# Performance work log

Measured on AMD Instinct MI355X. Metric: run time of the kernel, lower is better.

The kernel has to match this reference:

```python
import jax, jax.numpy as jnp
import numpy as np

EPS = 1e-5  # BatchNorm1d default eps

def _conv1d(x, w, stride, pad):
    # x: [B, Cin, L], w: [Cout, Cin, K]
    return jax.lax.conv_general_dilated(
        x, w, window_strides=(stride,), padding=[(pad, pad)],
        dimension_numbers=('NCH', 'OIH', 'NCH'))

def _bn(x, g, b, m, v):
    # eval-mode BatchNorm1d with running stats; x: [B, C, L]
    scale = g / jnp.sqrt(v + EPS)
    return x * scale[None, :, None] + (b - m * scale)[None, :, None]

def _hardtanh(x):
    return jnp.clip(x, -1.0, 1.0)

def _maxpool2(x):
    B, C, L = x.shape
    return x.reshape(B, C, L // 2, 2).max(axis=-1)


def setup_inputs() -> dict:
    key = jax.random.key(0)
    ks = jax.random.split(key, 20)
    B, L = 256, 16384
    x = jax.random.normal(ks[0], (B, 1, L), dtype=jnp.float32)
    rms = jax.random.uniform(ks[1], (B, 1), dtype=jnp.float32)
    # conv weights (fan-in scaled)
    w1 = jax.random.normal(ks[2], (16, 1, 17), dtype=jnp.float32) * (1.0 / np.sqrt(1 * 17))
    w2 = jax.random.normal(ks[3], (32, 16, 9), dtype=jnp.float32) * (1.0 / np.sqrt(16 * 9))
    w3 = jax.random.normal(ks[4], (64, 32, 5), dtype=jnp.float32) * (1.0 / np.sqrt(32 * 5))
    # batchnorm params (eval mode: gamma, beta, running mean/var)
    def bn_params(k, C):
        k1, k2, k3, k4 = jax.random.split(k, 4)
        g = 1.0 + 0.1 * jax.random.normal(k1, (C,), dtype=jnp.float32)
        b = 0.1 * jax.random.normal(k2, (C,), dtype=jnp.float32)
        m = 0.1 * jax.random.normal(k3, (C,), dtype=jnp.float32)
        v = jax.random.uniform(k4, (C,), dtype=jnp.float32, minval=0.5, maxval=1.5)
        return g, b, m, v
    g1, b1, m1, v1 = bn_params(ks[5], 16)
    g2, b2, m2, v2 = bn_params(ks[6], 32)
    g3, b3, m3, v3 = bn_params(ks[7], 64)
    fc1_w = jax.random.normal(ks[8], (32, 65), dtype=jnp.float32) * (1.0 / np.sqrt(65))
    fc1_b = jnp.zeros((32,), dtype=jnp.float32)
    fc2_w = jax.random.normal(ks[9], (2, 32), dtype=jnp.float32) * (1.0 / np.sqrt(32))
    fc2_b = jnp.zeros((2,), dtype=jnp.float32)
    return dict(x=x, rms=rms, w1=w1, g1=g1, b1=b1, m1=m1, v1=v1,
                w2=w2, g2=g2, b2=b2, m2=m2, v2=v2,
                w3=w3, g3=g3, b3=b3, m3=m3, v3=v3,
                fc1_w=fc1_w, fc1_b=fc1_b, fc2_w=fc2_w, fc2_b=fc2_b)


def reference(x, rms, w1, g1, b1, m1, v1, w2, g2, b2, m2, v2,
              w3, g3, b3, m3, v3, fc1_w, fc1_b, fc2_w, fc2_b):
    # Stage 1: float conv
    h = _conv1d(x, w1, 2, 8)                 # [B,16,8192]
    h = _maxpool2(_hardtanh(_bn(h, g1, b1, m1, v1)))  # [B,16,4096]
    # Stage 2: binarized (sign) weight conv
    h = _conv1d(h, jnp.sign(w2), 2, 4)       # [B,32,2048]
    h = _maxpool2(_hardtanh(_bn(h, g2, b2, m2, v2)))  # [B,32,1024]
    # Stage 3: binarized weight conv
    h = _conv1d(h, jnp.sign(w3), 2, 2)       # [B,64,512]
    h = _maxpool2(_hardtanh(_bn(h, g3, b3, m3, v3)))  # [B,64,256]
    feat = h.mean(axis=-1)                   # AdaptiveAvgPool1d(1) -> [B,64]
    combined = jnp.concatenate([feat, rms], axis=1)   # [B,65]
    h = _hardtanh(combined @ fc1_w.T + fc1_b)
    return h @ fc2_w.T + fc2_b               # [B,2]
```

## Files before the change

### kernel.cpp

```cpp
#include <hip/hip_runtime.h>
#include <hip/hip_bf16.h>

#define EPS 1e-5f

typedef float f32x4 __attribute__((ext_vector_type(4)));
typedef short s16x8 __attribute__((ext_vector_type(8)));

union FragU { uint4 u; s16x8 s; };

__device__ __forceinline__ float ht(float x){ return __builtin_amdgcn_fmed3f(x, -1.f, 1.f); }
__device__ __forceinline__ float sgn(float v){ return (v>0.f)?1.f:((v<0.f)?-1.f:0.f); }
__device__ __forceinline__ unsigned short f2bf(float f){
    unsigned int u = __builtin_bit_cast(unsigned int, f);
    u += 0x7FFFu + ((u>>16)&1u);
    return (unsigned short)(u>>16);
}
__device__ __forceinline__ unsigned pkbf(float a, float b){
    __hip_bfloat162 h = __float22bfloat162_rn(float2{a, b});
    unsigned u;
    __builtin_memcpy(&u, &h, sizeof(u));
    return u;
}

__global__ __launch_bounds__(512) void prep(
    const float* __restrict__ w1, const float* __restrict__ w2, const float* __restrict__ w3,
    const float* g1,const float* b1,const float* m1,const float* v1,
    const float* g2,const float* b2,const float* m2,const float* v2,
    const float* g3,const float* b3,const float* m3,const float* v3,
    unsigned short* __restrict__ a1, unsigned short* __restrict__ a2,
    unsigned short* __restrict__ a3, float* __restrict__ bn){
  const int t = threadIdx.x, bid = blockIdx.x;
  if(bid == 0){
    if(t < 64){
      int q = t>>4, m = t&15;
      #pragma unroll
      for(int j=0;j<8;++j){ int k = 8*q+j;
        a1[t*8+j] = f2bf((k<17)? w1[m*17+k] : 0.f); }
    }
    if(t<16){ float s = g1[t]*rsqrtf(v1[t]+EPS); bn[t]    = s; bn[16+t]  = b1[t]-m1[t]*s; }
    if(t<32){ float s = g2[t]*rsqrtf(v2[t]+EPS); bn[32+t] = s; bn[64+t]  = b2[t]-m2[t]*s; }
    if(t<64){ float s = g3[t]*rsqrtf(v3[t]+EPS); bn[96+t] = s; bn[160+t] = b3[t]-m3[t]*s; }
  } else if(bid <= 2){
    int e = (bid-1)*512 + t;
    if(e < 640){
      int m = e&15, q = (e>>4)&3, hc = e>>6, c = hc%5, h = hc/5;
      int oc = m + 16*h, k = 2*c + (q>>1);
      #pragma unroll
      for(int j=0;j<8;++j){ int ic = 8*(q&1)+j;
        a2[e*8+j] = f2bf((k<9)? sgn(w2[(oc*16+ic)*9+k]) : 0.f); }
    }
  } else {
    int e = (bid-3)*512 + t;
    if(e < 1280){
      int m = e&15, q = (e>>4)&3, gc = e>>6, c = gc%5, g = gc/5;
      int oc = m + 16*g;
      #pragma unroll
      for(int j=0;j<8;++j){ int ic = 8*q+j;
        a3[e*8+j] = f2bf(sgn(w3[(oc*32+ic)*5+c])); }
    }
  }
}

__global__ __launch_bounds__(256, 4) void kfused(const float* __restrict__ x,
    const unsigned short* __restrict__ a1, const unsigned short* __restrict__ a2,
    const unsigned short* __restrict__ a3, const float* __restrict__ bn,
    float* __restrict__ partial){
  __shared__ __align__(16) unsigned short xs[1216];
  __shared__ __align__(16) unsigned short s1[296*24];
  __shared__ __align__(16) unsigned short s2[68*40];
  __shared__ float fws[4*32];
  const int b  = blockIdx.x >> 4;
  const int t  = blockIdx.x & 15;
  const int Q0 = 16*t;
  const int tid = threadIdx.x;
  const int m = tid & 15, q = (tid & 63) >> 4, w = tid >> 6;

  const int x0 = 64*Q0 - 56;
  const float* xrow = &x[b*16384];
  for(int i = tid; i < 304; i += 256){
    int g0 = x0 + 4*i;
    float4 v = make_float4(0.f,0.f,0.f,0.f);
    if(g0 >= 0 && g0 <= 16380) v = *(const float4*)&xrow[g0];
    uint2 pk;
    pk.x = pkbf(v.x, v.y);
    pk.y = pkbf(v.z, v.w);
    *(uint2*)&xs[4*i] = pk;
  }
  FragU af1; af1.u = *(const uint4*)&a1[(q*16+m)*8];
  const float sc1 = bn[m], sh1 = bn[16+m];
  __syncthreads();

  const unsigned* X32 = (const unsigned*)xs;
  for(int it = 0; it < 10; ++it){
    int tile = it*4 + w;
    if(tile < 37){
      int d = tile*16 + m + 4*q;
      FragU bf;
      bf.u.x = X32[d]; bf.u.y = X32[d+1]; bf.u.z = X32[d+2]; bf.u.w = X32[d+3];
      f32x4 acc = {0.f,0.f,0.f,0.f};
      acc = __builtin_amdgcn_mfma_f32_16x16x32_bf16(bf.s, af1.s, acc, 0,0,0);
      float v0 = ht(acc[0]*sc1 + sh1);
      float v1 = ht(acc[1]*sc1 + sh1);
      float v2 = ht(acc[2]*sc1 + sh1);
      float v3 = ht(acc[3]*sc1 + sh1);
      int ppl = tile*8 + 2*q;
      int gp  = 16*Q0 - 12 + ppl;
      float p0 = ((unsigned)gp     < 4096u) ? fmaxf(v0, v1) : 0.f;
      float p1 = ((unsigned)(gp+1) < 4096u) ? fmaxf(v2, v3) : 0.f;
      unsigned u = pkbf(p0, p1);
      s1[ppl*24 + m]     = (unsigned short)u;
      s1[(ppl+1)*24 + m] = (unsigned short)(u >> 16);
    }
  }
  __syncthreads();

  FragU af2[2][5];
  #pragma unroll
  for(int h=0;h<2;++h)
    #pragma unroll
    for(int c=0;c<5;++c)
      af2[h][c].u = *(const uint4*)&a2[(((h*5+c)*4+q)*16+m)*8];
  float sc2[2], sh2[2];
  #pragma unroll
  for(int h=0;h<2;++h){
    sc2[h] = bn[32 + m + 16*h];
    sh2[h] = bn[64 + m + 16*h];
  }
  for(int it = 0; it < 3; ++it){
    int tile = it*4 + w;
    if(tile < 9){
      int nl = tile*16 + m;
      f32x4 acc[2] = {{0.f,0.f,0.f,0.f},{0.f,0.f,0.f,0.f}};
      #pragma unroll
      for(int c=0;c<5;++c){
        int row = 2*nl + 2*c + (q>>1);
        FragU bf; bf.u = *(const uint4*)&s1[row*24 + 8*(q&1)];
        acc[0] = __builtin_amdgcn_mfma_f32_16x16x32_bf16(bf.s, af2[0][c].s, acc[0],0,0,0);
        acc[1] = __builtin_amdgcn_mfma_f32_16x16x32_bf16(bf.s, af2[1][c].s, acc[1],0,0,0);
      }
      int ppl = tile*8 + 2*q;
      int gp  = 4*Q0 - 2 + ppl;
      bool ok0 = (unsigned)gp     < 1024u;
      bool ok1 = (unsigned)(gp+1) < 1024u;
      #pragma unroll
      for(int h=0;h<2;++h){
        float v0 = ht(acc[h][0]*sc2[h] + sh2[h]);
        float v1 = ht(acc[h][1]*sc2[h] + sh2[h]);
        float v2 = ht(acc[h][2]*sc2[h] + sh2[h]);
        float v3 = ht(acc[h][3]*sc2[h] + sh2[h]);
        float p0 = ok0 ? fmaxf(v0, v1) : 0.f;
        float p1 = ok1 ? fmaxf(v2, v3) : 0.f;
        unsigned u = pkbf(p0, p1);
        if(ppl < 68){
          s2[ppl*40 + m + 16*h]     = (unsigned short)u;
          s2[(ppl+1)*40 + m + 16*h] = (unsigned short)(u >> 16);
        }
      }
    }
  }
  __syncthreads();

  const int tw = w & 1, gw = w >> 1;
  FragU af3[2][5];
  #pragma unroll
  for(int gl=0;gl<2;++gl)
    #pragma unroll
    for(int c=0;c<5;++c)
      af3[gl][c].u = *(const uint4*)&a3[((((2*gw+gl)*5+c)*4+q)*16+m)*8];
  float sc3[2], sh3[2];
  #pragma unroll
  for(int gl=0;gl<2;++gl){
    sc3[gl] = bn[96  + m + 16*(2*gw+gl)];
    sh3[gl] = bn[160 + m + 16*(2*gw+gl)];
  }
  {
    int nl = tw*16 + m;
    f32x4 acc[2] = {{0.f,0.f,0.f,0.f},{0.f,0.f,0.f,0.f}};
    #pragma unroll
    for(int c=0;c<5;++c){
      int row = 2*nl + c;
      FragU bf; bf.u = *(const uint4*)&s2[row*40 + 8*q];
      acc[0] = __builtin_amdgcn_mfma_f32_16x16x32_bf16(bf.s, af3[0][c].s, acc[0],0,0,0);
      acc[1] = __builtin_amdgcn_mfma_f32_16x16x32_bf16(bf.s, af3[1][c].s, acc[1],0,0,0);
    }
    #pragma unroll
    for(int gl=0;gl<2;++gl){
      float v0 = ht(acc[gl][0]*sc3[gl] + sh3[gl]);
      float v1 = ht(acc[gl][1]*sc3[gl] + sh3[gl]);
      float v2 = ht(acc[gl][2]*sc3[gl] + sh3[gl]);
      float v3 = ht(acc[gl][3]*sc3[gl] + sh3[gl]);
      float sm = fmaxf(v0, v1) + fmaxf(v2, v3);
      sm += __shfl_xor(sm, 16);
      sm += __shfl_xor(sm, 32);
      if(q == 0) fws[w*32 + 16*gl + m] = sm;
    }
  }
  __syncthreads();
  if(tid < 64){
    int ocl = tid & 31, g = tid >> 5;
    float sum = fws[(2*g)*32 + ocl] + fws[(2*g+1)*32 + ocl];
    partial[(b*16 + t)*64 + tid] = sum;
  }
}

__global__ __launch_bounds__(64) void kfc(const float* __restrict__ partial,
    const float* __restrict__ rms, const float* __restrict__ fc1w,
    const float* __restrict__ fc1b, const float* __restrict__ fc2w,
    const float* __restrict__ fc2b, float* __restrict__ out){
  __shared__ float feat[64];
  __shared__ float hbuf[32];
  const int b = blockIdx.x, tid = threadIdx.x;
  float s = 0.f;
  #pragma unroll
  for(int t = 0; t < 16; ++t) s += partial[(b*16 + t)*64 + tid];
  feat[tid] = s * (1.f/256.f);
  __syncthreads();
  if(tid < 32){
    float acc = fc1b[tid];
    const float* wv = &fc1w[tid*65];
    #pragma unroll
    for(int c = 0; c < 64; ++c) acc += wv[c]*feat[c];
    acc += wv[64]*rms[b];
    hbuf[tid] = ht(acc);
  }
  __syncthreads();
  if(tid < 2){
    float acc = fc2b[tid];
    const float* wv = &fc2w[tid*32];
    #pragma unroll
    for(int j = 0; j < 32; ++j) acc += wv[j]*hbuf[j];
    out[b*2 + tid] = acc;
  }
}

extern "C" void kernel_launch(void* const* d_in, const int* in_sizes, int n_in,
                              void* d_out, int out_size, void* d_ws, size_t ws_size,
                              hipStream_t stream){
  (void)in_sizes; (void)n_in; (void)out_size; (void)ws_size;
  const float* x    = (const float*)d_in[0];
  const float* rms  = (const float*)d_in[1];
  const float* w1   = (const float*)d_in[2];
  const float* g1   = (const float*)d_in[3];
  const float* b1   = (const float*)d_in[4];
  const float* m1   = (const float*)d_in[5];
  const float* v1   = (const float*)d_in[6];
  const float* w2   = (const float*)d_in[7];
  const float* g2   = (const float*)d_in[8];
  const float* b2   = (const float*)d_in[9];
  const float* m2   = (const float*)d_in[10];
  const float* v2   = (const float*)d_in[11];
  const float* w3   = (const float*)d_in[12];
  const float* g3   = (const float*)d_in[13];
  const float* b3   = (const float*)d_in[14];
  const float* m3   = (const float*)d_in[15];
  const float* v3   = (const float*)d_in[16];
  const float* fc1w = (const float*)d_in[17];
  const float* fc1b = (const float*)d_in[18];
  const float* fc2w = (const float*)d_in[19];
  const float* fc2b = (const float*)d_in[20];
  float* out  = (float*)d_out;

  float*          partial = (float*)d_ws;
  unsigned short* a1  = (unsigned short*)(partial + 262144);
  unsigned short* a2  = a1 + 512;
  unsigned short* a3  = a2 + 5120;
  float*          bnp = (float*)(a3 + 10240);

  prep<<<6,    512, 0, stream>>>(w1, w2, w3, g1,b1,m1,v1, g2,b2,m2,v2, g3,b3,m3,v3,
                                 a1, a2, a3, bnp);
  kfused<<<4096, 256, 0, stream>>>(x, a1, a2, a3, bnp, partial);
  kfc<<<256, 64, 0, stream>>>(partial, rms, fc1w, fc1b, fc2w, fc2b, out);
}
```

Baseline: 123.8 us.

## Fuse FC head into conv kernel via last-block atomic counter, pad LDS rows

Removes the separate FC kernel launch. Each block bumps a per-batch atomic counter, and the last of the 16 tiles for that batch reduces the partial sums and evaluates the FC layers. The counter is zeroed in the prep kernel. LDS row strides go from 24/40 to 26/42 to cut bank conflicts, and launch bounds ask for 5 blocks per CU, which may increase register pressure or spilling. The threadfence and atomic add extra synchronisation cost to every block.

```diff
diff --git a/kernel.cpp b/kernel.cpp
--- a/kernel.cpp
+++ b/kernel.cpp
@@ -28,7 +28,8 @@
     const float* g2,const float* b2,const float* m2,const float* v2,
     const float* g3,const float* b3,const float* m3,const float* v3,
     unsigned short* __restrict__ a1, unsigned short* __restrict__ a2,
-    unsigned short* __restrict__ a3, float* __restrict__ bn){
+    unsigned short* __restrict__ a3, float* __restrict__ bn,
+    unsigned* __restrict__ cnt){
   const int t = threadIdx.x, bid = blockIdx.x;
   if(bid == 0){
     if(t < 64){
@@ -40,6 +41,7 @@
     if(t<16){ float s = g1[t]*rsqrtf(v1[t]+EPS); bn[t]    = s; bn[16+t]  = b1[t]-m1[t]*s; }
     if(t<32){ float s = g2[t]*rsqrtf(v2[t]+EPS); bn[32+t] = s; bn[64+t]  = b2[t]-m2[t]*s; }
     if(t<64){ float s = g3[t]*rsqrtf(v3[t]+EPS); bn[96+t] = s; bn[160+t] = b3[t]-m3[t]*s; }
+    if(t<256) cnt[t] = 0u;
   } else if(bid <= 2){
     int e = (bid-1)*512 + t;
     if(e < 640){
@@ -61,14 +63,19 @@
   }
 }
 
-__global__ __launch_bounds__(256, 4) void kfused(const float* __restrict__ x,
+__global__ __launch_bounds__(256, 5) void kfused(const float* __restrict__ x,
     const unsigned short* __restrict__ a1, const unsigned short* __restrict__ a2,
     const unsigned short* __restrict__ a3, const float* __restrict__ bn,
-    float* __restrict__ partial){
+    float* __restrict__ partial, unsigned* __restrict__ cnt,
+    const float* __restrict__ rms, const float* __restrict__ fc1w,
+    const float* __restrict__ fc1b, const float* __restrict__ fc2w,
+    const float* __restrict__ fc2b, float* __restrict__ out){
   __shared__ __align__(16) unsigned short xs[1216];
-  __shared__ __align__(16) unsigned short s1[296*24];
-  __shared__ __align__(16) unsigned short s2[68*40];
+  __shared__ __align__(16) unsigned short s1[296*26];
+  __shared__ __align__(16) unsigned short s2[68*42];
   __shared__ float fws[4*32];
+  __shared__ float fcb[96];
+  __shared__ int flg;
   const int b  = blockIdx.x >> 4;
   const int t  = blockIdx.x & 15;
   const int Q0 = 16*t;
@@ -108,8 +115,8 @@
       float p0 = ((unsigned)gp     < 4096u) ? fmaxf(v0, v1) : 0.f;
       float p1 = ((unsigned)(gp+1) < 4096u) ? fmaxf(v2, v3) : 0.f;
       unsigned u = pkbf(p0, p1);
-      s1[ppl*24 + m]     = (unsigned short)u;
-      s1[(ppl+1)*24 + m] = (unsigned short)(u >> 16);
+      s1[ppl*26 + m]     = (unsigned short)u;
+      s1[(ppl+1)*26 + m] = (unsigned short)(u >> 16);
     }
   }
   __syncthreads();
@@ -134,7 +141,7 @@
       #pragma unroll
       for(int c=0;c<5;++c){
         int row = 2*nl + 2*c + (q>>1);
-        FragU bf; bf.u = *(const uint4*)&s1[row*24 + 8*(q&1)];
+        FragU bf; bf.u = *(const uint4*)&s1[row*26 + 8*(q&1)];
         acc[0] = __builtin_amdgcn_mfma_f32_16x16x32_bf16(bf.s, af2[0][c].s, acc[0],0,0,0);
         acc[1] = __builtin_amdgcn_mfma_f32_16x16x32_bf16(bf.s, af2[1][c].s, acc[1],0,0,0);
       }
@@ -152,8 +159,8 @@
         float p1 = ok1 ? fmaxf(v2, v3) : 0.f;
         unsigned u = pkbf(p0, p1);
         if(ppl < 68){
-          s2[ppl*40 + m + 16*h]     = (unsigned short)u;
-          s2[(ppl+1)*40 + m + 16*h] = (unsigned short)(u >> 16);
+          s2[ppl*42 + m + 16*h]     = (unsigned short)u;
+          s2[(ppl+1)*42 + m + 16*h] = (unsigned short)(u >> 16);
         }
       }
     }
@@ -179,7 +186,7 @@
     #pragma unroll
     for(int c=0;c<5;++c){
       int row = 2*nl + c;
-      FragU bf; bf.u = *(const uint4*)&s2[row*40 + 8*q];
+      FragU bf; bf.u = *(const uint4*)&s2[row*42 + 8*q];
       acc[0] = __builtin_amdgcn_mfma_f32_16x16x32_bf16(bf.s, af3[0][c].s, acc[0],0,0,0);
       acc[1] = __builtin_amdgcn_mfma_f32_16x16x32_bf16(bf.s, af3[1][c].s, acc[1],0,0,0);
     }
@@ -201,35 +208,38 @@
     float sum = fws[(2*g)*32 + ocl] + fws[(2*g+1)*32 + ocl];
     partial[(b*16 + t)*64 + tid] = sum;
   }
-}
-
-__global__ __launch_bounds__(64) void kfc(const float* __restrict__ partial,
-    const float* __restrict__ rms, const float* __restrict__ fc1w,
-    const float* __restrict__ fc1b, const float* __restrict__ fc2w,
-    const float* __restrict__ fc2b, float* __restrict__ out){
-  __shared__ float feat[64];
-  __shared__ float hbuf[32];
-  const int b = blockIdx.x, tid = threadIdx.x;
-  float s = 0.f;
-  #pragma unroll
-  for(int t = 0; t < 16; ++t) s += partial[(b*16 + t)*64 + tid];
-  feat[tid] = s * (1.f/256.f);
-  __syncthreads();
-  if(tid < 32){
-    float acc = fc1b[tid];
-    const float* wv = &fc1w[tid*65];
-    #pragma unroll
-    for(int c = 0; c < 64; ++c) acc += wv[c]*feat[c];
-    acc += wv[64]*rms[b];
-    hbuf[tid] = ht(acc);
-  }
-  __syncthreads();
-  if(tid < 2){
-    float acc = fc2b[tid];
-    const float* wv = &fc2w[tid*32];
-    #pragma unroll
-    for(int j = 0; j < 32; ++j) acc += wv[j]*hbuf[j];
-    out[b*2 + tid] = acc;
+  __threadfence();
+  __syncthreads();
+  if(tid == 0){
+    unsigned old = __hip_atomic_fetch_add(&cnt[b], 1u,
+                                          __ATOMIC_ACQ_REL, __HIP_MEMORY_SCOPE_AGENT);
+    flg = (old == 15u);
+  }
+  __syncthreads();
+  if(flg){
+    if(tid < 64){
+      float s = 0.f;
+      #pragma unroll
+      for(int tt = 0; tt < 16; ++tt) s += partial[(b*16 + tt)*64 + tid];
+      fcb[tid] = s * (1.f/256.f);
+    }
+    __syncthreads();
+    if(tid < 32){
+      float acc = fc1b[tid];
+      const float* wv = &fc1w[tid*65];
+      #pragma unroll
+      for(int c = 0; c < 64; ++c) acc += wv[c]*fcb[c];
+      acc += wv[64]*rms[b];
+      fcb[64+tid] = ht(acc);
+    }
+    __syncthreads();
+    if(tid < 2){
+      float acc = fc2b[tid];
+      const float* wv = &fc2w[tid*32];
+      #pragma unroll
+      for(int j = 0; j < 32; ++j) acc += wv[j]*fcb[64+j];
+      out[b*2 + tid] = acc;
+    }
   }
 }
 
@@ -265,9 +275,10 @@
   unsigned short* a2  = a1 + 512;
   unsigned short* a3  = a2 + 5120;
   float*          bnp = (float*)(a3 + 10240);
+  unsigned*       cnt = (unsigned*)(bnp + 224);
 
   prep<<<6,    512, 0, stream>>>(w1, w2, w3, g1,b1,m1,v1, g2,b2,m2,v2, g3,b3,m3,v3,
-                                 a1, a2, a3, bnp);
-  kfused<<<4096, 256, 0, stream>>>(x, a1, a2, a3, bnp, partial);
-  kfc<<<256, 64, 0, stream>>>(partial, rms, fc1w, fc1b, fc2w, fc2b, out);
-}
+                                 a1, a2, a3, bnp, cnt);
+  kfused<<<4096, 256, 0, stream>>>(x, a1, a2, a3, bnp, partial, cnt,
+                                   rms, fc1w, fc1b, fc2w, fc2b, out);
+}
```

After: 467.3 us. 277% more time.
